# Optimization experiments

Measured on AMD Instinct MI355X. Metric: run time of the kernel, lower is better.

## Reference

```python
import jax, jax.numpy as jnp
import numpy as np
from jax import lax

N, GH, GE, LH, LL = 19, 64, 64, 64, 2
B, T = 256, 256


def _normalized_adjacency(A):
    # A: (..., n, n). Add self-loops, symmetric degree normalization.
    n = A.shape[-1]
    A = A + jnp.eye(n, dtype=A.dtype)
    deg = jnp.clip(A.sum(axis=-1), 1e-6, None)  # (..., n)
    dis = deg ** -0.5
    return A * dis[..., :, None] * dis[..., None, :]


def _graph_encoder(A, w1_w, w1_b, w2_w, w2_b):
    # A: (B, T, n, n) -> (B, T, GE). Node features X = A rows.
    An = _normalized_adjacency(A)
    X = jax.nn.relu(An @ (A @ w1_w.T + w1_b))   # (B,T,n,GH)
    X = jax.nn.relu(An @ (X @ w2_w.T + w2_b))   # (B,T,n,GE)
    return X.mean(axis=-2)


def _lstm_layer(x, Wih, Whh, bih, bhh):
    # x: (B, T, D); PyTorch gate order i,f,g,o. Returns (B, T, H).
    Bb = x.shape[0]
    H = Whh.shape[1]
    xg = x @ Wih.T + (bih + bhh)  # precompute input contributions (B,T,4H)

    def step(carry, xt):
        h, c = carry
        gates = xt + h @ Whh.T
        i, f, g, o = jnp.split(gates, 4, axis=-1)
        c = jax.nn.sigmoid(f) * c + jax.nn.sigmoid(i) * jnp.tanh(g)
        h = jax.nn.sigmoid(o) * jnp.tanh(c)
        return (h, c), h

    h0 = jnp.zeros((Bb, H), x.dtype)
    (_, _), hs = lax.scan(step, (h0, h0), jnp.swapaxes(xg, 0, 1))
    return jnp.swapaxes(hs, 0, 1)


def setup_inputs() -> dict:
    key = jax.random.key(0)
    ks = jax.random.split(key, 20)
    s = 0.1
    inp = {
        'conn': jax.random.uniform(ks[0], (B, T, N, N), jnp.float32),
        'mask': jnp.ones((B, T), jnp.int32),
        'w1_w': jax.random.normal(ks[1], (GH, N), jnp.float32) * s,
        'w1_b': jax.random.normal(ks[2], (GH,), jnp.float32) * s,
        'w2_w': jax.random.normal(ks[3], (GE, GH), jnp.float32) * s,
        'w2_b': jax.random.normal(ks[4], (GE,), jnp.float32) * s,
        'lstm_Wih0': jax.random.normal(ks[5], (4 * LH, GE), jnp.float32) * s,
        'lstm_Whh0': jax.random.normal(ks[6], (4 * LH, LH), jnp.float32) * s,
        'lstm_bih0': jax.random.normal(ks[7], (4 * LH,), jnp.float32) * s,
        'lstm_bhh0': jax.random.normal(ks[8], (4 * LH,), jnp.float32) * s,
        'lstm_Wih1': jax.random.normal(ks[9], (4 * LH, LH), jnp.float32) * s,
        'lstm_Whh1': jax.random.normal(ks[10], (4 * LH, LH), jnp.float32) * s,
        'lstm_bih1': jax.random.normal(ks[11], (4 * LH,), jnp.float32) * s,
        'lstm_bhh1': jax.random.normal(ks[12], (4 * LH,), jnp.float32) * s,
        'fc1_w': jax.random.normal(ks[13], (32, LH), jnp.float32) * s,
        'fc1_b': jax.random.normal(ks[14], (32,), jnp.float32) * s,
        'fc2_w': jax.random.normal(ks[15], (2, 32), jnp.float32) * s,
        'fc2_b': jax.random.normal(ks[16], (2,), jnp.float32) * s,
    }
    return inp


def reference(conn, mask, w1_w, w1_b, w2_w, w2_b,
              lstm_Wih0, lstm_Whh0, lstm_bih0, lstm_bhh0,
              lstm_Wih1, lstm_Whh1, lstm_bih1, lstm_bhh1,
              fc1_w, fc1_b, fc2_w, fc2_b):
    emb = _graph_encoder(conn, w1_w, w1_b, w2_w, w2_b)  # (B,T,GE)
    mf = mask.astype(emb.dtype)
    emb = emb * mf[:, :, None]
    out = _lstm_layer(emb, lstm_Wih0, lstm_Whh0, lstm_bih0, lstm_bhh0)
    out = _lstm_layer(out, lstm_Wih1, lstm_Whh1, lstm_bih1, lstm_bhh1)  # (B,T,LH)
    lengths = jnp.clip(mask.sum(axis=1), 1, None)
    last_idx = jnp.clip(lengths - 1, 0, None)  # (B,)
    last_h = jnp.take_along_axis(out, last_idx[:, None, None], axis=1)[:, 0, :]
    h = jax.nn.relu(last_h @ fc1_w.T + fc1_b)
    return h @ fc2_w.T + fc2_b  # (B,2) logits
```

## Files before the change

kernel.cpp:

```cpp
#include <hip/hip_runtime.h>
#include <hip/hip_bf16.h>
#include <math.h>

#define GN 19
#define BB 256
#define TT 256

typedef short short8 __attribute__((ext_vector_type(8)));
typedef float f4 __attribute__((ext_vector_type(4)));

union Frag { int i[4]; short8 s; };

#define LWAIT() __asm__ volatile("s_waitcnt lgkmcnt(0)" ::: "memory")
#define WGBAR() __asm__ volatile("s_waitcnt lgkmcnt(0)\ns_barrier" ::: "memory")

#define MFMA(a,b,c) __builtin_amdgcn_mfma_f32_16x16x32_bf16(a,b,c,0,0,0)

__device__ __forceinline__ int pkbf(float a, float b) {
    __hip_bfloat162 h2 = __float22bfloat162_rn(make_float2(a, b));
    union { __hip_bfloat162 h; int i; } u; u.h = h2; return u.i;
}

__device__ __forceinline__ float fexp2(float x) { return __builtin_amdgcn_exp2f(x); }
__device__ __forceinline__ float frcp(float x)  { return __builtin_amdgcn_rcpf(x); }
__device__ __forceinline__ float sigm(float x)  { return frcp(1.f + fexp2(-1.4426950408889634f * x)); }
__device__ __forceinline__ float tanha(float x) { float e = fexp2(2.8853900817779268f * x); return 1.f - 2.f * frcp(e + 1.f); }

__global__ __launch_bounds__(64) void encoder_mfma(
    const float* __restrict__ conn,
    const int*   __restrict__ mask,
    const float* __restrict__ w1_w,
    const float* __restrict__ w1_b,
    const float* __restrict__ w2_w,
    const float* __restrict__ w2_b,
    float* __restrict__ emb,
    int num_graphs)
{
    __shared__ float S[2304];
    __shared__ float dis[32];
    __shared__ float ps[256];

    const int t = threadIdx.x;
    const int l15 = t & 15;
    const int quad = t >> 4;

    float km[8];
    #pragma unroll
    for (int j = 0; j < 8; ++j) km[j] = (quad * 8 + j < GN) ? 1.f : 0.f;

    int rr[6], cc[6];
    #pragma unroll
    for (int i = 0; i < 6; ++i) {
        int e = t + 64 * i;
        rr[i] = e / GN;
        cc[i] = e - rr[i] * GN;
    }

    Frag w1F[4];
    #pragma unroll
    for (int nt = 0; nt < 4; ++nt) {
        int n = nt * 16 + l15;
        #pragma unroll
        for (int p = 0; p < 4; ++p) {
            int k0 = quad * 8 + 2 * p, k1 = k0 + 1;
            float a = (k0 < GN) ? w1_w[n * GN + k0] : 0.f;
            float b = (k1 < GN) ? w1_w[n * GN + k1] : 0.f;
            w1F[nt].i[p] = pkbf(a, b);
        }
    }
    Frag w2F[2][4];
    #pragma unroll
    for (int kt = 0; kt < 2; ++kt)
        #pragma unroll
        for (int nt = 0; nt < 4; ++nt) {
            int n = nt * 16 + l15;
            #pragma unroll
            for (int p = 0; p < 4; ++p) {
                int k = kt * 32 + quad * 8 + 2 * p;
                w2F[kt][nt].i[p] = pkbf(w2_w[n * 64 + k], w2_w[n * 64 + k + 1]);
            }
        }
    float b1v[4], b2v[4];
    #pragma unroll
    for (int nt = 0; nt < 4; ++nt) {
        b1v[nt] = w1_b[nt * 16 + l15];
        b2v[nt] = w2_b[nt * 16 + l15];
    }

    float pf[6];
    {
        int g0 = blockIdx.x < num_graphs ? blockIdx.x : 0;
        const float* Ag = conn + (size_t)g0 * (GN * GN);
        #pragma unroll
        for (int i = 0; i < 6; ++i) {
            int e = t + 64 * i;
            if (e < GN * GN) pf[i] = Ag[e];
        }
    }

    #pragma unroll 1
    for (int g = blockIdx.x; g < num_graphs; g += gridDim.x) {
        #pragma unroll
        for (int i = 0; i < 4; ++i) {
            int s = t + 64 * i;
            int row = s >> 3, c4 = s & 7;
            f4 z = {0.f, 0.f, 0.f, 0.f};
            *(f4*)&S[row * 68 + c4 * 4] = z;
        }
        LWAIT();
        #pragma unroll
        for (int i = 0; i < 6; ++i) {
            if (t + 64 * i < GN * GN) S[rr[i] * 68 + cc[i]] = pf[i];
        }
        {
            int gn = g + gridDim.x;
            const float* Ag = conn + (size_t)(gn < num_graphs ? gn : g) * (GN * GN);
            #pragma unroll
            for (int i = 0; i < 6; ++i) {
                int e = t + 64 * i;
                if (e < GN * GN) pf[i] = Ag[e];
            }
        }
        LWAIT();

        if (t < 32) {
            float dv = 0.f;
            if (t < GN) {
                float d = 1.0f;
                #pragma unroll
                for (int c4 = 0; c4 < 8; ++c4) {
                    f4 v = *(f4*)&S[t * 68 + c4 * 4];
                    d += v.x + v.y + v.z + v.w;
                }
                dv = rsqrtf(d);
            }
            dis[t] = dv;
        }
        LWAIT();

        float dk[8];
        {
            f4 v0 = *(f4*)&dis[quad * 8];
            f4 v1 = *(f4*)&dis[quad * 8 + 4];
            dk[0]=v0.x; dk[1]=v0.y; dk[2]=v0.z; dk[3]=v0.w;
            dk[4]=v1.x; dk[5]=v1.y; dk[6]=v1.z; dk[7]=v1.w;
        }
        Frag aF[2], anF[2];
        #pragma unroll
        for (int mt = 0; mt < 2; ++mt) {
            int m = l15 + 16 * mt;
            float dm = dis[m];
            f4 v0 = *(f4*)&S[m * 68 + quad * 8];
            f4 v1 = *(f4*)&S[m * 68 + quad * 8 + 4];
            float av[8] = {v0.x, v0.y, v0.z, v0.w, v1.x, v1.y, v1.z, v1.w};
            float an[8];
            #pragma unroll
            for (int j = 0; j < 8; ++j) {
                int k = quad * 8 + j;
                an[j] = (av[j] + (m == k ? 1.f : 0.f)) * dm * dk[j];
            }
            #pragma unroll
            for (int p = 0; p < 4; ++p) {
                aF[mt].i[p]  = pkbf(av[2*p], av[2*p+1]);
                anF[mt].i[p] = pkbf(an[2*p], an[2*p+1]);
            }
        }
        LWAIT();

        #pragma unroll
        for (int mt = 0; mt < 2; ++mt)
            #pragma unroll
            for (int nt = 0; nt < 4; ++nt) {
                float bb = b1v[nt];
                f4 c = {bb, bb, bb, bb};
                c = MFMA(aF[mt].s, w1F[nt].s, c);
                int col = nt * 16 + l15;
                #pragma unroll
                for (int r = 0; r < 4; ++r)
                    S[col * 36 + (mt * 16 + quad * 4 + r)] = c[r];
            }
        LWAIT();

        Frag hF[4];
        #pragma unroll
        for (int nt = 0; nt < 4; ++nt) {
            int n = nt * 16 + l15;
            f4 v0 = *(f4*)&S[n * 36 + quad * 8];
            f4 v1 = *(f4*)&S[n * 36 + quad * 8 + 4];
            float vv[8] = {v0.x, v0.y, v0.z, v0.w, v1.x, v1.y, v1.z, v1.w};
            #pragma unroll
            for (int p = 0; p < 4; ++p)
                hF[nt].i[p] = pkbf(vv[2*p] * km[2*p], vv[2*p+1] * km[2*p+1]);
        }
        LWAIT();

        #pragma unroll
        for (int mt = 0; mt < 2; ++mt)
            #pragma unroll
            for (int nt = 0; nt < 4; ++nt) {
                f4 c = {0.f, 0.f, 0.f, 0.f};
                c = MFMA(anF[mt].s, hF[nt].s, c);
                int col = nt * 16 + l15;
                #pragma unroll
                for (int r = 0; r < 4; ++r)
                    S[(mt * 16 + quad * 4 + r) * 68 + col] = fmaxf(c[r], 0.f);
            }
        LWAIT();

        Frag xF[2][2];
        #pragma unroll
        for (int mt = 0; mt < 2; ++mt) {
            int m = l15 + 16 * mt;
            #pragma unroll
            for (int kt = 0; kt < 2; ++kt) {
                f4 v0 = *(f4*)&S[m * 68 + kt * 32 + quad * 8];
                f4 v1 = *(f4*)&S[m * 68 + kt * 32 + quad * 8 + 4];
                xF[mt][kt].i[0] = pkbf(v0.x, v0.y);
                xF[mt][kt].i[1] = pkbf(v0.z, v0.w);
                xF[mt][kt].i[2] = pkbf(v1.x, v1.y);
                xF[mt][kt].i[3] = pkbf(v1.z, v1.w);
            }
        }
        LWAIT();

        #pragma unroll
        for (int mt = 0; mt < 2; ++mt)
            #pragma unroll
            for (int nt = 0; nt < 4; ++nt) {
                float bb = b2v[nt];
                f4 c = {bb, bb, bb, bb};
                c = MFMA(xF[mt][0].s, w2F[0][nt].s, c);
                c = MFMA(xF[mt][1].s, w2F[1][nt].s, c);
                int col = nt * 16 + l15;
                #pragma unroll
                for (int r = 0; r < 4; ++r)
                    S[col * 36 + (mt * 16 + quad * 4 + r)] = c[r];
            }
        LWAIT();

        Frag hG[4];
        #pragma unroll
        for (int nt = 0; nt < 4; ++nt) {
            int n = nt * 16 + l15;
            f4 v0 = *(f4*)&S[n * 36 + quad * 8];
            f4 v1 = *(f4*)&S[n * 36 + quad * 8 + 4];
            float vv[8] = {v0.x, v0.y, v0.z, v0.w, v1.x, v1.y, v1.z, v1.w};
            #pragma unroll
            for (int p = 0; p < 4; ++p)
                hG[nt].i[p] = pkbf(vv[2*p] * km[2*p], vv[2*p+1] * km[2*p+1]);
        }

        float cs[4];
        #pragma unroll
        for (int nt = 0; nt < 4; ++nt) cs[nt] = 0.f;
        #pragma unroll
        for (int mt = 0; mt < 2; ++mt)
            #pragma unroll
            for (int nt = 0; nt < 4; ++nt) {
                f4 c = {0.f, 0.f, 0.f, 0.f};
                c = MFMA(anF[mt].s, hG[nt].s, c);
                if (mt == 0) {
                    cs[nt] += fmaxf(c[0], 0.f) + fmaxf(c[1], 0.f)
                            + fmaxf(c[2], 0.f) + fmaxf(c[3], 0.f);
                } else if (quad == 0) {
                    cs[nt] += fmaxf(c[0], 0.f) + fmaxf(c[1], 0.f) + fmaxf(c[2], 0.f);
                }
            }
        #pragma unroll
        for (int nt = 0; nt < 4; ++nt)
            ps[quad * 64 + nt * 16 + l15] = cs[nt];
        LWAIT();
        float tot = ps[t] + ps[64 + t] + ps[128 + t] + ps[192 + t];
        float mf = (float)mask[g];
        emb[(size_t)g * 64 + t] = tot * (1.f / 19.f) * mf;
        LWAIT();
    }
}

__global__ __launch_bounds__(512, 2) void lstm_mfma(
    const float* __restrict__ x,
    const int*   __restrict__ mask,
    const float* __restrict__ Wih0, const float* __restrict__ Whh0,
    const float* __restrict__ bih0, const float* __restrict__ bhh0,
    const float* __restrict__ Wih1, const float* __restrict__ Whh1,
    const float* __restrict__ bih1, const float* __restrict__ bhh1,
    const float* __restrict__ fc1_w, const float* __restrict__ fc1_b,
    const float* __restrict__ fc2_w, const float* __restrict__ fc2_b,
    float* __restrict__ out)
{
    __shared__ int   h0b[2][16 * 68];
    __shared__ int   h1b[2][16 * 68];
    __shared__ float hlast[16][68];
    __shared__ float red[512];
    __shared__ int   li_s[16];

    const int tid  = threadIdx.x;
    const int w    = tid >> 6;
    const int lane = tid & 63;
    const int l15  = lane & 15;
    const int quad = lane >> 4;
    const int bb0  = blockIdx.x * 16;

    {
        int b16 = tid >> 5, j = tid & 31;
        int s = 0;
        #pragma unroll
        for (int c8 = 0; c8 < 8; ++c8)
            s += mask[(bb0 + b16) * TT + j + 32 * c8];
        red[tid] = (float)s;
    }
    __syncthreads();
    if (tid < 16) {
        float s = 0.f;
        #pragma unroll
        for (int j = 0; j < 32; ++j) s += red[tid * 32 + j];
        int li = (int)s - 1;
        li_s[tid] = li < 0 ? 0 : (li > TT - 1 ? TT - 1 : li);
    }
    __syncthreads();
    const int li = li_s[l15];

    Frag Aih0[2][2], Ahh0[2][2], Aih1[2][2], Ahh1[2][2];
    f4 bias0v[2], bias1v[2];
    #pragma unroll
    for (int mt = 0; mt < 2; ++mt) {
        int mg = 2 * w + mt;
        int orig = (l15 & 3) * 64 + (mg * 4 + (l15 >> 2));
        #pragma unroll
        for (int kt = 0; kt < 2; ++kt)
            #pragma unroll
            for (int p = 0; p < 4; ++p) {
                int k = kt * 32 + quad * 8 + 2 * p;
                Aih0[mt][kt].i[p] = pkbf(Wih0[orig * 64 + k], Wih0[orig * 64 + k + 1]);
                Ahh0[mt][kt].i[p] = pkbf(Whh0[orig * 64 + k], Whh0[orig * 64 + k + 1]);
                Aih1[mt][kt].i[p] = pkbf(Wih1[orig * 64 + k], Wih1[orig * 64 + k + 1]);
                Ahh1[mt][kt].i[p] = pkbf(Whh1[orig * 64 + k], Whh1[orig * 64 + k + 1]);
            }
        int uu = mg * 4 + quad;
        #pragma unroll
        for (int r = 0; r < 4; ++r) {
            bias0v[mt][r] = bih0[r * 64 + uu] + bhh0[r * 64 + uu];
            bias1v[mt][r] = bih1[r * 64 + uu] + bhh1[r * 64 + uu];
        }
    }
    const int uoff0 = (2 * w + 0) * 4 + quad;
    const int uoff1 = (2 * w + 1) * 4 + quad;

    Frag BX[2], BH0h[2], BH0l[2], BH1h[2], BH1l[2];
    #pragma unroll
    for (int kt = 0; kt < 2; ++kt)
        #pragma unroll
        for (int p = 0; p < 4; ++p) {
            BX[kt].i[p] = 0; BH0h[kt].i[p] = 0; BH0l[kt].i[p] = 0;
            BH1h[kt].i[p] = 0; BH1l[kt].i[p] = 0;
        }
    float c0s[2] = {0.f, 0.f}, c1s[2] = {0.f, 0.f}, h1last[2] = {0.f, 0.f};

    const float* __restrict__ xb = x + (size_t)(bb0 + l15) * TT * 64;
    f4 xpre[4];
    {
        const f4* p0 = (const f4*)(xb + quad * 8);
        const f4* p1 = (const f4*)(xb + 32 + quad * 8);
        xpre[0] = p0[0]; xpre[1] = p0[1];
        xpre[2] = p1[0]; xpre[3] = p1[1];
    }

    #pragma unroll 1
    for (int it = 0; it <= TT; ++it) {
        const int cur = it & 1;

        if (it < TT) {
            #pragma unroll
            for (int kt = 0; kt < 2; ++kt) {
                f4 v0 = xpre[kt * 2], v1 = xpre[kt * 2 + 1];
                BX[kt].i[0] = pkbf(v0.x, v0.y);
                BX[kt].i[1] = pkbf(v0.z, v0.w);
                BX[kt].i[2] = pkbf(v1.x, v1.y);
                BX[kt].i[3] = pkbf(v1.z, v1.w);
            }
            int tn = it + 1 < TT ? it + 1 : TT - 1;
            const f4* p0 = (const f4*)(xb + (size_t)tn * 64 + quad * 8);
            const f4* p1 = (const f4*)(xb + (size_t)tn * 64 + 32 + quad * 8);
            xpre[0] = p0[0]; xpre[1] = p0[1];
            xpre[2] = p1[0]; xpre[3] = p1[1];
        }

        f4 g0[2], g1[2];
        if (it < TT) {
            #pragma unroll
            for (int mt = 0; mt < 2; ++mt) {
                f4 c = bias0v[mt];
                c = MFMA(Aih0[mt][0].s, BX[0].s,   c);
                c = MFMA(Aih0[mt][1].s, BX[1].s,   c);
                c = MFMA(Ahh0[mt][0].s, BH0h[0].s, c);
                c = MFMA(Ahh0[mt][1].s, BH0h[1].s, c);
                c = MFMA(Ahh0[mt][0].s, BH0l[0].s, c);
                c = MFMA(Ahh0[mt][1].s, BH0l[1].s, c);
                g0[mt] = c;
            }
        }
        if (it >= 1) {
            #pragma unroll
            for (int mt = 0; mt < 2; ++mt) {
                f4 c = bias1v[mt];
                c = MFMA(Aih1[mt][0].s, BH0h[0].s, c);
                c = MFMA(Aih1[mt][1].s, BH0h[1].s, c);
                c = MFMA(Aih1[mt][0].s, BH0l[0].s, c);
                c = MFMA(Aih1[mt][1].s, BH0l[1].s, c);
                c = MFMA(Ahh1[mt][0].s, BH1h[0].s, c);
                c = MFMA(Ahh1[mt][1].s, BH1h[1].s, c);
                c = MFMA(Ahh1[mt][0].s, BH1l[0].s, c);
                c = MFMA(Ahh1[mt][1].s, BH1l[1].s, c);
                g1[mt] = c;
            }
        }

        if (it < TT) {
            #pragma unroll
            for (int mt = 0; mt < 2; ++mt) {
                f4 g = g0[mt];
                float si = sigm(g[0]), sf = sigm(g[1]);
                float tg = tanha(g[2]), so = sigm(g[3]);
                float cc = fmaf(sf, c0s[mt], si * tg);
                c0s[mt] = cc;
                float h = so * tanha(cc);
                unsigned hb = __float_as_uint(h);
                float hhi = __uint_as_float(hb & 0xFFFF0000u);
                float hlo = h - hhi;
                unsigned lopk = (unsigned)pkbf(hlo, hlo);
                int packed = (int)__builtin_amdgcn_perm(lopk, hb, 0x05040302u);
                h0b[cur][l15 * 68 + (mt ? uoff1 : uoff0)] = packed;
            }
        }
        if (it >= 1) {
            #pragma unroll
            for (int mt = 0; mt < 2; ++mt) {
                f4 g = g1[mt];
                float si = sigm(g[0]), sf = sigm(g[1]);
                float tg = tanha(g[2]), so = sigm(g[3]);
                float cc = fmaf(sf, c1s[mt], si * tg);
                c1s[mt] = cc;
                float h = so * tanha(cc);
                if (it - 1 == li) h1last[mt] = h;
                unsigned hb = __float_as_uint(h);
                float hhi = __uint_as_float(hb & 0xFFFF0000u);
                float hlo = h - hhi;
                unsigned lopk = (unsigned)pkbf(hlo, hlo);
                int packed = (int)__builtin_amdgcn_perm(lopk, hb, 0x05040302u);
                h1b[cur][l15 * 68 + (mt ? uoff1 : uoff0)] = packed;
            }
        }

        WGBAR();

        if (it < TT) {
            #pragma unroll
            for (int kt = 0; kt < 2; ++kt) {
                const int4* pp = (const int4*)&h0b[cur][l15 * 68 + kt * 32 + quad * 8];
                int4 va = pp[0], vb = pp[1];
                BH0h[kt].i[0] = (int)__builtin_amdgcn_perm((unsigned)va.y, (unsigned)va.x, 0x05040100u);
                BH0h[kt].i[1] = (int)__builtin_amdgcn_perm((unsigned)va.w, (unsigned)va.z, 0x05040100u);
                BH0h[kt].i[2] = (int)__builtin_amdgcn_perm((unsigned)vb.y, (unsigned)vb.x, 0x05040100u);
                BH0h[kt].i[3] = (int)__builtin_amdgcn_perm((unsigned)vb.w, (unsigned)vb.z, 0x05040100u);
                BH0l[kt].i[0] = (int)__builtin_amdgcn_perm((unsigned)va.y, (unsigned)va.x, 0x07060302u);
                BH0l[kt].i[1] = (int)__builtin_amdgcn_perm((unsigned)va.w, (unsigned)va.z, 0x07060302u);
                BH0l[kt].i[2] = (int)__builtin_amdgcn_perm((unsigned)vb.y, (unsigned)vb.x, 0x07060302u);
                BH0l[kt].i[3] = (int)__builtin_amdgcn_perm((unsigned)vb.w, (unsigned)vb.z, 0x07060302u);
            }
            if (it >= 1) {
                #pragma unroll
                for (int kt = 0; kt < 2; ++kt) {
                    const int4* pp = (const int4*)&h1b[cur][l15 * 68 + kt * 32 + quad * 8];
                    int4 va = pp[0], vb = pp[1];
                    BH1h[kt].i[0] = (int)__builtin_amdgcn_perm((unsigned)va.y, (unsigned)va.x, 0x05040100u);
                    BH1h[kt].i[1] = (int)__builtin_amdgcn_perm((unsigned)va.w, (unsigned)va.z, 0x05040100u);
                    BH1h[kt].i[2] = (int)__builtin_amdgcn_perm((unsigned)vb.y, (unsigned)vb.x, 0x05040100u);
                    BH1h[kt].i[3] = (int)__builtin_amdgcn_perm((unsigned)vb.w, (unsigned)vb.z, 0x05040100u);
                    BH1l[kt].i[0] = (int)__builtin_amdgcn_perm((unsigned)va.y, (unsigned)va.x, 0x07060302u);
                    BH1l[kt].i[1] = (int)__builtin_amdgcn_perm((unsigned)va.w, (unsigned)va.z, 0x07060302u);
                    BH1l[kt].i[2] = (int)__builtin_amdgcn_perm((unsigned)vb.y, (unsigned)vb.x, 0x07060302u);
                    BH1l[kt].i[3] = (int)__builtin_amdgcn_perm((unsigned)vb.w, (unsigned)vb.z, 0x07060302u);
                }
            }
        }
    }

    hlast[l15][uoff0] = h1last[0];
    hlast[l15][uoff1] = h1last[1];
    __syncthreads();
    {
        int b = tid >> 5, o = tid & 31;
        float acc = fc1_b[o];
        const float* fw = fc1_w + o * 64;
        #pragma unroll
        for (int j = 0; j < 64; ++j)
            acc = fmaf(hlast[b][j], fw[j], acc);
        red[b * 32 + o] = fmaxf(acc, 0.f);
    }
    __syncthreads();
    if (tid < 32) {
        int b = tid >> 1, o = tid & 1;
        float acc = fc2_b[o];
        #pragma unroll
        for (int j = 0; j < 32; ++j)
            acc = fmaf(fc2_w[o * 32 + j], red[b * 32 + j], acc);
        out[(bb0 + b) * 2 + o] = acc;
    }
}

extern "C" void kernel_launch(void* const* d_in, const int* in_sizes, int n_in,
                              void* d_out, int out_size, void* d_ws, size_t ws_size,
                              hipStream_t stream)
{
    const float* conn  = (const float*)d_in[0];
    const int*   mask  = (const int*)  d_in[1];
    const float* w1_w  = (const float*)d_in[2];
    const float* w1_b  = (const float*)d_in[3];
    const float* w2_w  = (const float*)d_in[4];
    const float* w2_b  = (const float*)d_in[5];
    const float* Wih0  = (const float*)d_in[6];
    const float* Whh0  = (const float*)d_in[7];
    const float* bih0  = (const float*)d_in[8];
    const float* bhh0  = (const float*)d_in[9];
    const float* Wih1  = (const float*)d_in[10];
    const float* Whh1  = (const float*)d_in[11];
    const float* bih1  = (const float*)d_in[12];
    const float* bhh1  = (const float*)d_in[13];
    const float* fc1_w = (const float*)d_in[14];
    const float* fc1_b = (const float*)d_in[15];
    const float* fc2_w = (const float*)d_in[16];
    const float* fc2_b = (const float*)d_in[17];

    float* out = (float*)d_out;
    float* emb = (float*)d_ws;

    const int num_graphs = BB * TT;

    encoder_mfma<<<8192, 64, 0, stream>>>(
        conn, mask, w1_w, w1_b, w2_w, w2_b, emb, num_graphs);

    lstm_mfma<<<16, 512, 0, stream>>>(
        emb, mask, Wih0, Whh0, bih0, bhh0, Wih1, Whh1, bih1, bhh1,
        fc1_w, fc1_b, fc2_w, fc2_b, out);
}
```

Baseline: 615.2 us.

## Split LSTM layers across two wave groups in a 1024-thread block

The LSTM kernel now runs with 1024 threads, with waves 0-7 handling layer 0 and waves 8-15 handling layer 1 as a wavefront pipeline. Each wave then holds only its own layer's weights, which lowers register pressure. The K-dimension MFMA chain is split into two independent accumulators to shorten dependency latency. The cost is a barrier across twice as many waves every timestep, and layer 1 still waits on layer 0 through shared memory.

```diff
diff --git a/kernel.cpp b/kernel.cpp
--- a/kernel.cpp
+++ b/kernel.cpp
@@ -13,6 +13,8 @@
 
 #define LWAIT() __asm__ volatile("s_waitcnt lgkmcnt(0)" ::: "memory")
 #define WGBAR() __asm__ volatile("s_waitcnt lgkmcnt(0)\ns_barrier" ::: "memory")
+#define PIN8(x) __asm__ volatile("" : "+v"(x))
+#define PINF(x) __asm__ volatile("" : "+v"(x))
 
 #define MFMA(a,b,c) __builtin_amdgcn_mfma_f32_16x16x32_bf16(a,b,c,0,0,0)
 
@@ -277,7 +279,27 @@
     }
 }
 
-__global__ __launch_bounds__(512, 2) void lstm_mfma(
+__device__ __forceinline__ void unpack_h(const int* __restrict__ src,
+                                         int l15, int quad,
+                                         Frag* __restrict__ BHh,
+                                         Frag* __restrict__ BHl)
+{
+    #pragma unroll
+    for (int kt = 0; kt < 2; ++kt) {
+        const int4* pp = (const int4*)&src[l15 * 68 + kt * 32 + quad * 8];
+        int4 va = pp[0], vb = pp[1];
+        BHh[kt].i[0] = (int)__builtin_amdgcn_perm((unsigned)va.y, (unsigned)va.x, 0x05040100u);
+        BHh[kt].i[1] = (int)__builtin_amdgcn_perm((unsigned)va.w, (unsigned)va.z, 0x05040100u);
+        BHh[kt].i[2] = (int)__builtin_amdgcn_perm((unsigned)vb.y, (unsigned)vb.x, 0x05040100u);
+        BHh[kt].i[3] = (int)__builtin_amdgcn_perm((unsigned)vb.w, (unsigned)vb.z, 0x05040100u);
+        BHl[kt].i[0] = (int)__builtin_amdgcn_perm((unsigned)va.y, (unsigned)va.x, 0x07060302u);
+        BHl[kt].i[1] = (int)__builtin_amdgcn_perm((unsigned)va.w, (unsigned)va.z, 0x07060302u);
+        BHl[kt].i[2] = (int)__builtin_amdgcn_perm((unsigned)vb.y, (unsigned)vb.x, 0x07060302u);
+        BHl[kt].i[3] = (int)__builtin_amdgcn_perm((unsigned)vb.w, (unsigned)vb.z, 0x07060302u);
+    }
+}
+
+__global__ __launch_bounds__(1024, 4) void lstm_mfma(
     const float* __restrict__ x,
     const int*   __restrict__ mask,
     const float* __restrict__ Wih0, const float* __restrict__ Whh0,
@@ -296,12 +318,16 @@
 
     const int tid  = threadIdx.x;
     const int w    = tid >> 6;
+    const int grp  = w >> 3;
+    const int wl   = w & 7;
     const int lane = tid & 63;
     const int l15  = lane & 15;
     const int quad = lane >> 4;
     const int bb0  = blockIdx.x * 16;
 
-    {
+    for (int i = tid; i < 16 * 68; i += 1024) h1b[0][i] = 0;
+
+    if (tid < 512) {
         int b16 = tid >> 5, j = tid & 31;
         int s = 0;
         #pragma unroll
@@ -320,31 +346,39 @@
     __syncthreads();
     const int li = li_s[l15];
 
-    Frag Aih0[2][2], Ahh0[2][2], Aih1[2][2], Ahh1[2][2];
-    f4 bias0v[2], bias1v[2];
+    const float* __restrict__ Wx = grp ? Wih1 : Wih0;
+    const float* __restrict__ Wh = grp ? Whh1 : Whh0;
+    const float* __restrict__ bi = grp ? bih1 : bih0;
+    const float* __restrict__ bh = grp ? bhh1 : bhh0;
+
+    Frag Ax[2][2], Ah[2][2];
+    f4 biasv[2];
     #pragma unroll
     for (int mt = 0; mt < 2; ++mt) {
-        int mg = 2 * w + mt;
+        int mg = 2 * wl + mt;
         int orig = (l15 & 3) * 64 + (mg * 4 + (l15 >> 2));
         #pragma unroll
         for (int kt = 0; kt < 2; ++kt)
             #pragma unroll
             for (int p = 0; p < 4; ++p) {
                 int k = kt * 32 + quad * 8 + 2 * p;
-                Aih0[mt][kt].i[p] = pkbf(Wih0[orig * 64 + k], Wih0[orig * 64 + k + 1]);
-                Ahh0[mt][kt].i[p] = pkbf(Whh0[orig * 64 + k], Whh0[orig * 64 + k + 1]);
-                Aih1[mt][kt].i[p] = pkbf(Wih1[orig * 64 + k], Wih1[orig * 64 + k + 1]);
-                Ahh1[mt][kt].i[p] = pkbf(Whh1[orig * 64 + k], Whh1[orig * 64 + k + 1]);
+                Ax[mt][kt].i[p] = pkbf(Wx[orig * 64 + k], Wx[orig * 64 + k + 1]);
+                Ah[mt][kt].i[p] = pkbf(Wh[orig * 64 + k], Wh[orig * 64 + k + 1]);
             }
         int uu = mg * 4 + quad;
         #pragma unroll
-        for (int r = 0; r < 4; ++r) {
-            bias0v[mt][r] = bih0[r * 64 + uu] + bhh0[r * 64 + uu];
-            bias1v[mt][r] = bih1[r * 64 + uu] + bhh1[r * 64 + uu];
-        }
-    }
-    const int uoff0 = (2 * w + 0) * 4 + quad;
-    const int uoff1 = (2 * w + 1) * 4 + quad;
+        for (int r = 0; r < 4; ++r)
+            biasv[mt][r] = bi[r * 64 + uu] + bh[r * 64 + uu];
+    }
+    #pragma unroll
+    for (int mt = 0; mt < 2; ++mt) {
+        PIN8(Ax[mt][0].s); PIN8(Ax[mt][1].s);
+        PIN8(Ah[mt][0].s); PIN8(Ah[mt][1].s);
+        PINF(biasv[mt]);
+    }
+
+    const int u0 = (2 * wl + 0) * 4 + quad;
+    const int u1 = (2 * wl + 1) * 4 + quad;
 
     Frag BX[2], BH0h[2], BH0l[2], BH1h[2], BH1l[2];
     #pragma unroll
@@ -354,11 +388,11 @@
             BX[kt].i[p] = 0; BH0h[kt].i[p] = 0; BH0l[kt].i[p] = 0;
             BH1h[kt].i[p] = 0; BH1l[kt].i[p] = 0;
         }
-    float c0s[2] = {0.f, 0.f}, c1s[2] = {0.f, 0.f}, h1last[2] = {0.f, 0.f};
+    float cst[2] = {0.f, 0.f}, hlv[2] = {0.f, 0.f};
 
     const float* __restrict__ xb = x + (size_t)(bb0 + l15) * TT * 64;
     f4 xpre[4];
-    {
+    if (grp == 0) {
         const f4* p0 = (const f4*)(xb + quad * 8);
         const f4* p1 = (const f4*)(xb + 32 + quad * 8);
         xpre[0] = p0[0]; xpre[1] = p0[1];
@@ -368,127 +402,93 @@
     #pragma unroll 1
     for (int it = 0; it <= TT; ++it) {
         const int cur = it & 1;
-
-        if (it < TT) {
-            #pragma unroll
-            for (int kt = 0; kt < 2; ++kt) {
-                f4 v0 = xpre[kt * 2], v1 = xpre[kt * 2 + 1];
-                BX[kt].i[0] = pkbf(v0.x, v0.y);
-                BX[kt].i[1] = pkbf(v0.z, v0.w);
-                BX[kt].i[2] = pkbf(v1.x, v1.y);
-                BX[kt].i[3] = pkbf(v1.z, v1.w);
-            }
-            int tn = it + 1 < TT ? it + 1 : TT - 1;
-            const f4* p0 = (const f4*)(xb + (size_t)tn * 64 + quad * 8);
-            const f4* p1 = (const f4*)(xb + (size_t)tn * 64 + 32 + quad * 8);
-            xpre[0] = p0[0]; xpre[1] = p0[1];
-            xpre[2] = p1[0]; xpre[3] = p1[1];
-        }
-
-        f4 g0[2], g1[2];
-        if (it < TT) {
+        f4 g[2];
+        bool act = false;
+
+        if (grp == 0) {
+            if (it < TT) {
+                act = true;
+                #pragma unroll
+                for (int kt = 0; kt < 2; ++kt) {
+                    f4 v0 = xpre[kt * 2], v1 = xpre[kt * 2 + 1];
+                    BX[kt].i[0] = pkbf(v0.x, v0.y);
+                    BX[kt].i[1] = pkbf(v0.z, v0.w);
+                    BX[kt].i[2] = pkbf(v1.x, v1.y);
+                    BX[kt].i[3] = pkbf(v1.z, v1.w);
+                }
+                int tn = it + 1 < TT ? it + 1 : TT - 1;
+                const f4* p0 = (const f4*)(xb + (size_t)tn * 64 + quad * 8);
+                const f4* p1 = (const f4*)(xb + (size_t)tn * 64 + 32 + quad * 8);
+                xpre[0] = p0[0]; xpre[1] = p0[1];
+                xpre[2] = p1[0]; xpre[3] = p1[1];
+
+                #pragma unroll
+                for (int mt = 0; mt < 2; ++mt) {
+                    f4 ca = biasv[mt];
+                    ca = MFMA(Ax[mt][0].s, BX[0].s,   ca);
+                    ca = MFMA(Ah[mt][0].s, BH0h[0].s, ca);
+                    ca = MFMA(Ah[mt][0].s, BH0l[0].s, ca);
+                    f4 cb = {0.f, 0.f, 0.f, 0.f};
+                    cb = MFMA(Ax[mt][1].s, BX[1].s,   cb);
+                    cb = MFMA(Ah[mt][1].s, BH0h[1].s, cb);
+                    cb = MFMA(Ah[mt][1].s, BH0l[1].s, cb);
+                    g[mt] = ca + cb;
+                }
+            }
+        } else {
+            if (it >= 1) {
+                act = true;
+                #pragma unroll
+                for (int mt = 0; mt < 2; ++mt) {
+                    f4 ca = biasv[mt];
+                    ca = MFMA(Ax[mt][0].s, BH0h[0].s, ca);
+                    ca = MFMA(Ax[mt][0].s, BH0l[0].s, ca);
+                    ca = MFMA(Ah[mt][0].s, BH1h[0].s, ca);
+                    ca = MFMA(Ah[mt][0].s, BH1l[0].s, ca);
+                    f4 cb = {0.f, 0.f, 0.f, 0.f};
+                    cb = MFMA(Ax[mt][1].s, BH0h[1].s, cb);
+                    cb = MFMA(Ax[mt][1].s, BH0l[1].s, cb);
+                    cb = MFMA(Ah[mt][1].s, BH1h[1].s, cb);
+                    cb = MFMA(Ah[mt][1].s, BH1l[1].s, cb);
+                    g[mt] = ca + cb;
+                }
+            }
+        }
+
+        if (act) {
+            int* __restrict__ dst = grp ? h1b[cur] : h0b[cur];
             #pragma unroll
             for (int mt = 0; mt < 2; ++mt) {
-                f4 c = bias0v[mt];
-                c = MFMA(Aih0[mt][0].s, BX[0].s,   c);
-                c = MFMA(Aih0[mt][1].s, BX[1].s,   c);
-                c = MFMA(Ahh0[mt][0].s, BH0h[0].s, c);
-                c = MFMA(Ahh0[mt][1].s, BH0h[1].s, c);
-                c = MFMA(Ahh0[mt][0].s, BH0l[0].s, c);
-                c = MFMA(Ahh0[mt][1].s, BH0l[1].s, c);
-                g0[mt] = c;
-            }
-        }
-        if (it >= 1) {
-            #pragma unroll
-            for (int mt = 0; mt < 2; ++mt) {
-                f4 c = bias1v[mt];
-                c = MFMA(Aih1[mt][0].s, BH0h[0].s, c);
-                c = MFMA(Aih1[mt][1].s, BH0h[1].s, c);
-                c = MFMA(Aih1[mt][0].s, BH0l[0].s, c);
-                c = MFMA(Aih1[mt][1].s, BH0l[1].s, c);
-                c = MFMA(Ahh1[mt][0].s, BH1h[0].s, c);
-                c = MFMA(Ahh1[mt][1].s, BH1h[1].s, c);
-                c = MFMA(Ahh1[mt][0].s, BH1l[0].s, c);
-                c = MFMA(Ahh1[mt][1].s, BH1l[1].s, c);
-                g1[mt] = c;
-            }
-        }
-
-        if (it < TT) {
-            #pragma unroll
-            for (int mt = 0; mt < 2; ++mt) {
-                f4 g = g0[mt];
-                float si = sigm(g[0]), sf = sigm(g[1]);
-                float tg = tanha(g[2]), so = sigm(g[3]);
-                float cc = fmaf(sf, c0s[mt], si * tg);
-                c0s[mt] = cc;
+                f4 gg = g[mt];
+                float si = sigm(gg[0]), sf = sigm(gg[1]);
+                float tg = tanha(gg[2]), so = sigm(gg[3]);
+                float cc = fmaf(sf, cst[mt], si * tg);
+                cst[mt] = cc;
                 float h = so * tanha(cc);
+                if (grp && it - 1 == li) hlv[mt] = h;
                 unsigned hb = __float_as_uint(h);
                 float hhi = __uint_as_float(hb & 0xFFFF0000u);
                 float hlo = h - hhi;
                 unsigned lopk = (unsigned)pkbf(hlo, hlo);
                 int packed = (int)__builtin_amdgcn_perm(lopk, hb, 0x05040302u);
-                h0b[cur][l15 * 68 + (mt ? uoff1 : uoff0)] = packed;
-            }
-        }
-        if (it >= 1) {
-            #pragma unroll
-            for (int mt = 0; mt < 2; ++mt) {
-                f4 g = g1[mt];
-                float si = sigm(g[0]), sf = sigm(g[1]);
-                float tg = tanha(g[2]), so = sigm(g[3]);
-                float cc = fmaf(sf, c1s[mt], si * tg);
-                c1s[mt] = cc;
-                float h = so * tanha(cc);
-                if (it - 1 == li) h1last[mt] = h;
-                unsigned hb = __float_as_uint(h);
-                float hhi = __uint_as_float(hb & 0xFFFF0000u);
-                float hlo = h - hhi;
-                unsigned lopk = (unsigned)pkbf(hlo, hlo);
-                int packed = (int)__builtin_amdgcn_perm(lopk, hb, 0x05040302u);
-                h1b[cur][l15 * 68 + (mt ? uoff1 : uoff0)] = packed;
+                dst[l15 * 68 + (mt ? u1 : u0)] = packed;
             }
         }
 
         WGBAR();
 
         if (it < TT) {
-            #pragma unroll
-            for (int kt = 0; kt < 2; ++kt) {
-                const int4* pp = (const int4*)&h0b[cur][l15 * 68 + kt * 32 + quad * 8];
-                int4 va = pp[0], vb = pp[1];
-                BH0h[kt].i[0] = (int)__builtin_amdgcn_perm((unsigned)va.y, (unsigned)va.x, 0x05040100u);
-                BH0h[kt].i[1] = (int)__builtin_amdgcn_perm((unsigned)va.w, (unsigned)va.z, 0x05040100u);
-                BH0h[kt].i[2] = (int)__builtin_amdgcn_perm((unsigned)vb.y, (unsigned)vb.x, 0x05040100u);
-                BH0h[kt].i[3] = (int)__builtin_amdgcn_perm((unsigned)vb.w, (unsigned)vb.z, 0x05040100u);
-                BH0l[kt].i[0] = (int)__builtin_amdgcn_perm((unsigned)va.y, (unsigned)va.x, 0x07060302u);
-                BH0l[kt].i[1] = (int)__builtin_amdgcn_perm((unsigned)va.w, (unsigned)va.z, 0x07060302u);
-                BH0l[kt].i[2] = (int)__builtin_amdgcn_perm((unsigned)vb.y, (unsigned)vb.x, 0x07060302u);
-                BH0l[kt].i[3] = (int)__builtin_amdgcn_perm((unsigned)vb.w, (unsigned)vb.z, 0x07060302u);
-            }
-            if (it >= 1) {
-                #pragma unroll
-                for (int kt = 0; kt < 2; ++kt) {
-                    const int4* pp = (const int4*)&h1b[cur][l15 * 68 + kt * 32 + quad * 8];
-                    int4 va = pp[0], vb = pp[1];
-                    BH1h[kt].i[0] = (int)__builtin_amdgcn_perm((unsigned)va.y, (unsigned)va.x, 0x05040100u);
-                    BH1h[kt].i[1] = (int)__builtin_amdgcn_perm((unsigned)va.w, (unsigned)va.z, 0x05040100u);
-                    BH1h[kt].i[2] = (int)__builtin_amdgcn_perm((unsigned)vb.y, (unsigned)vb.x, 0x05040100u);
-                    BH1h[kt].i[3] = (int)__builtin_amdgcn_perm((unsigned)vb.w, (unsigned)vb.z, 0x05040100u);
-                    BH1l[kt].i[0] = (int)__builtin_amdgcn_perm((unsigned)va.y, (unsigned)va.x, 0x07060302u);
-                    BH1l[kt].i[1] = (int)__builtin_amdgcn_perm((unsigned)va.w, (unsigned)va.z, 0x07060302u);
-                    BH1l[kt].i[2] = (int)__builtin_amdgcn_perm((unsigned)vb.y, (unsigned)vb.x, 0x07060302u);
-                    BH1l[kt].i[3] = (int)__builtin_amdgcn_perm((unsigned)vb.w, (unsigned)vb.z, 0x07060302u);
-                }
-            }
-        }
-    }
-
-    hlast[l15][uoff0] = h1last[0];
-    hlast[l15][uoff1] = h1last[1];
+            unpack_h(h0b[cur], l15, quad, BH0h, BH0l);
+            if (grp) unpack_h(h1b[cur], l15, quad, BH1h, BH1l);
+        }
+    }
+
+    if (grp == 1) {
+        hlast[l15][u0] = hlv[0];
+        hlast[l15][u1] = hlv[1];
+    }
     __syncthreads();
-    {
+    if (tid < 512) {
         int b = tid >> 5, o = tid & 31;
         float acc = fc1_b[o];
         const float* fw = fc1_w + o * 64;
@@ -539,7 +539,7 @@
     encoder_mfma<<<8192, 64, 0, stream>>>(
         conn, mask, w1_w, w1_b, w2_w, w2_b, emb, num_graphs);
 
-    lstm_mfma<<<16, 512, 0, stream>>>(
+    lstm_mfma<<<16, 1024, 0, stream>>>(
         emb, mask, Wih0, Whh0, bih0, bhh0, Wih1, Whh1, bih1, bhh1,
         fc1_w, fc1_b, fc2_w, fc2_b, out);
 }
```

After: 603.8 us. Within noise of the previous version (-1.9%).
